# Kernel optimization log

Hardware: AMD Instinct MI355X
Metric: run time of the kernel (lower is better)

The kernel has to match this reference:

```python
import jax, jax.numpy as jnp
import numpy as np

NUM_CLASSES = 2
KS = 5  # kernel_size
EPS = 1e-8  # torch cosine_similarity eps


def setup_inputs() -> dict:
    key = jax.random.key(0)
    k1, k2, k3 = jax.random.split(key, 3)
    b, c, h, w = 8, 256, 128, 128
    er_input = jax.random.normal(k1, (b, c, h, w), dtype=jnp.float32)
    seg_label = jax.random.randint(k2, (b, h, w), 0, 2, dtype=jnp.int32)
    gt_boundary_seg = jax.random.randint(k3, (b, h, w), 0, 2, dtype=jnp.int32)
    return {"er_input": er_input, "seg_label": seg_label, "gt_boundary_seg": gt_boundary_seg}


def _context_loss(er_input, seg_label, gt_boundary_seg):
    # seg_label / gt_boundary_seg already at er_input spatial size (nearest interp is identity)
    b, c, h, w = er_input.shape
    r = KS // 2
    seg0 = jnp.where(seg_label == 255, 0, seg_label)
    gtb0 = jnp.where(gt_boundary_seg == 255, 0, gt_boundary_seg)
    gt_b = gtb0 * seg0                                  # [b,h,w] boundary pixels on fg classes
    interior = jnp.zeros((h, w), bool).at[r:h - r, r:w - r].set(True)
    valid = (gt_b > 0) & interior                       # pixels whose 5x5 window is in-bounds
    include = (gt_b > 0).any(axis=(1, 2))               # images contributing to scale_num
    cnt = valid.sum(axis=(1, 2)).astype(er_input.dtype)  # [b]

    norm = jnp.maximum(jnp.sqrt((er_input * er_input).sum(axis=1)), EPS)  # [b,h,w]
    validf = valid.astype(er_input.dtype)
    total = jnp.zeros((b,), dtype=er_input.dtype)
    n_shift = 0
    for dy in range(-r, r + 1):
        for dx in range(-r, r + 1):
            if dy == 0 and dx == 0:
                continue
            n_shift += 1
            # value at p+ (dy,dx) brought to p; valid pixels are interior so no wrap issue
            feat_s = jnp.roll(er_input, (-dy, -dx), axis=(2, 3))
            norm_s = jnp.roll(norm, (-dy, -dx), axis=(1, 2))
            seg_s = jnp.roll(seg_label, (-dy, -dx), axis=(1, 2))
            dot = (er_input * feat_s).sum(axis=1)       # [b,h,w]
            cos = dot / (norm * norm_s)
            # one_hot(seg,256)[:num_classes] dot product == labels equal AND label < num_classes
            labsim = ((seg_label == seg_s) & (seg_label < NUM_CLASSES)).astype(er_input.dtype)
            sq = (cos - labsim) ** 2
            # mse_loss over selected boundary pixels of image i
            total = total + (sq * validf).sum(axis=(1, 2)) / jnp.maximum(cnt, 1.0)
    loss_i = total / float(n_shift)                     # per-image context_loss_pi / 24
    scale_num = jnp.maximum(include.sum(), 1)
    return (loss_i * include.astype(loss_i.dtype)).sum() / scale_num.astype(loss_i.dtype)


def reference(er_input, seg_label, gt_boundary_seg):
    return _context_loss(er_input, seg_label, gt_boundary_seg)
```

## Files before the change

kernel.cpp:

```cpp
#include <hip/hip_runtime.h>
#include <math.h>

#define BATCH 8
#define CH    256
#define H     128
#define W     128
#define PLANE (H * W)
#define NPIX  (BATCH * PLANE)
#define NSHIFT 12
#define NMAPS  13
#define NCHUNK 8
#define CPC    (CH / NCHUNK)
#define SLICE  (NMAPS * NPIX)

static __device__ __constant__ int S_DY[NSHIFT] = {0,0,1,1,1,1,1,2,2,2,2,2};
static __device__ __constant__ int S_DX[NSHIFT] = {1,2,-2,-1,0,1,2,-2,-1,0,1,2};

#define NCORRB (BATCH * 32 * NCHUNK)
#define NSTATB (BATCH * 64)

__device__ __forceinline__ void fma4(float& acc, const float4& a, const float4& b) {
    acc = fmaf(a.x, b.x, acc);
    acc = fmaf(a.y, b.y, acc);
    acc = fmaf(a.z, b.z, acc);
    acc = fmaf(a.w, b.w, acc);
}

__global__ void k_prep(int* __restrict__ cnt, int* __restrict__ inc,
                       float* __restrict__ out) {
    int t = threadIdx.x;
    if (t < 8) { cnt[t] = 0; inc[t] = 0; }
    if (t == 0) out[0] = 0.0f;
}

__global__ __launch_bounds__(256) void k_corr(const float* __restrict__ er,
                                              const int* __restrict__ seg,
                                              const int* __restrict__ gtb,
                                              float* __restrict__ slices,
                                              int* __restrict__ cnt,
                                              int* __restrict__ inc) {
    __shared__ float4 lds[6][132];
    int t = threadIdx.x;

    if (blockIdx.x >= NCORRB) {
        int blk2 = blockIdx.x - NCORRB;
        int b = blk2 >> 6;
        int i = (blk2 & 63) * 256 + t;
        int my_cnt = 0, my_any = 0;
        {
            int s = seg[b * PLANE + i];
            int g = gtb[b * PLANE + i];
            int s0 = (s == 255) ? 0 : s;
            int g0 = (g == 255) ? 0 : g;
            if (s0 > 0 && g0 > 0) {
                my_any = 1;
                int y = i >> 7, x = i & 127;
                if (y >= 2 && y < H - 2 && x >= 2 && x < W - 2) my_cnt = 1;
            }
        }
        for (int o = 32; o > 0; o >>= 1) {
            my_cnt += __shfl_down(my_cnt, o, 64);
            my_any |= __shfl_down(my_any, o, 64);
        }
        __shared__ int sc[4], sa[4];
        int lane = t & 63, wid = t >> 6;
        if (lane == 0) { sc[wid] = my_cnt; sa[wid] = my_any; }
        __syncthreads();
        if (t == 0) {
            int c = sc[0] + sc[1] + sc[2] + sc[3];
            int a = sa[0] | sa[1] | sa[2] | sa[3];
            if (c) atomicAdd(&cnt[b], c);
            if (a) atomicOr(&inc[b], 1);
        }
        return;
    }

    int blk = blockIdx.x;
    int chunk = blk & 7;
    int tile  = (blk >> 3) & 31;
    int b     = blk >> 8;
    int y0 = tile * 4;
    int c0 = chunk * CPC;
    int r = t >> 7;
    int x = t & 127;

    if (t < 24) {
        int row = t >> 2, col = t & 3;
        int xs = (col < 2) ? col : (col + 128);
        lds[row][xs] = make_float4(0.f, 0.f, 0.f, 0.f);
    }

    float accA[13], accB[13];
#pragma unroll
    for (int i = 0; i < 13; i++) { accA[i] = 0.0f; accB[i] = 0.0f; }

    const float* base = er + (size_t)b * CH * PLANE;

    float pf[3][4];
    auto load_quad = [&](int c) {
#pragma unroll
        for (int k = 0; k < 3; ++k) {
            int s = t + k * 256;
            int row = s >> 7;
            int xs = s & 127;
            int y = y0 + row;
            if (y < H) {
                const float* p0 = base + (size_t)c * PLANE + y * W + xs;
                pf[k][0] = p0[0];
                pf[k][1] = p0[PLANE];
                pf[k][2] = p0[2 * PLANE];
                pf[k][3] = p0[3 * PLANE];
            } else {
                pf[k][0] = 0.f; pf[k][1] = 0.f; pf[k][2] = 0.f; pf[k][3] = 0.f;
            }
        }
    };

    load_quad(c0);
    const int iters = CPC / 4;
    for (int it = 0; it < iters; ++it) {
        __syncthreads();
#pragma unroll
        for (int k = 0; k < 3; ++k) {
            int s = t + k * 256;
            int row = s >> 7;
            int xs = s & 127;
            lds[row][xs + 2] = make_float4(pf[k][0], pf[k][1], pf[k][2], pf[k][3]);
        }
        __syncthreads();
        if (it + 1 < iters) load_quad(c0 + 4 * (it + 1));

        const float4* lp = &lds[2 * r][x + 2];
        float4 cA = lp[0];
        float4 cB = lp[132];
        {
            float4 v1 = lp[1], v2 = lp[2];
            fma4(accA[0], cA, cA);
            fma4(accA[1], cA, v1);
            fma4(accA[2], cA, v2);
        }
        {
            float4 m2 = lp[130], m1 = lp[131], p1 = lp[133], p2 = lp[134];
            fma4(accA[3], cA, m2);
            fma4(accA[4], cA, m1);
            fma4(accA[5], cA, cB);
            fma4(accA[6], cA, p1);
            fma4(accA[7], cA, p2);
            fma4(accB[0], cB, cB);
            fma4(accB[1], cB, p1);
            fma4(accB[2], cB, p2);
        }
        {
            float4 m2 = lp[262], m1 = lp[263], v0 = lp[264], p1 = lp[265], p2 = lp[266];
            fma4(accA[8],  cA, m2);
            fma4(accA[9],  cA, m1);
            fma4(accA[10], cA, v0);
            fma4(accA[11], cA, p1);
            fma4(accA[12], cA, p2);
            fma4(accB[3], cB, m2);
            fma4(accB[4], cB, m1);
            fma4(accB[5], cB, v0);
            fma4(accB[6], cB, p1);
            fma4(accB[7], cB, p2);
        }
        {
            float4 m2 = lp[394], m1 = lp[395], v0 = lp[396], p1 = lp[397], p2 = lp[398];
            fma4(accB[8],  cB, m2);
            fma4(accB[9],  cB, m1);
            fma4(accB[10], cB, v0);
            fma4(accB[11], cB, p1);
            fma4(accB[12], cB, p2);
        }
    }

    float* sp = slices + (size_t)chunk * SLICE;
    int pixA = b * PLANE + (y0 + 2 * r) * W + x;
    int pixB = pixA + W;
#pragma unroll
    for (int m = 0; m < NSHIFT; ++m) {
        sp[m * NPIX + pixA] = accA[m + 1];
        sp[m * NPIX + pixB] = accB[m + 1];
    }
    sp[NSHIFT * NPIX + pixA] = accA[0];
    sp[NSHIFT * NPIX + pixB] = accB[0];
}

__global__ __launch_bounds__(256) void k_combine(const float4* __restrict__ sl,
                                                 float4* __restrict__ comb) {
    int i = blockIdx.x * 256 + threadIdx.x;
    float4 s = sl[i];
#pragma unroll
    for (int c = 1; c < NCHUNK; ++c) {
        float4 v = sl[(size_t)c * (SLICE / 4) + i];
        s.x += v.x; s.y += v.y; s.z += v.z; s.w += v.w;
    }
    comb[i] = s;
}

__global__ __launch_bounds__(256) void k_loss(const float* __restrict__ comb,
                                              const int* __restrict__ seg,
                                              const int* __restrict__ gtb,
                                              const int* __restrict__ cnt,
                                              const int* __restrict__ inc,
                                              float* __restrict__ out) {
    const float* dots   = comb;
    const float* normsq = comb + NSHIFT * NPIX;
    int idx = blockIdx.x * 256 + threadIdx.x;
    int b = idx >> 14;
    int rem = idx & (PLANE - 1);
    int y = rem >> 7;
    int x = rem & 127;

    int sn = 0;
#pragma unroll
    for (int b2 = 0; b2 < BATCH; b2++) sn += (inc[b2] != 0);
    if (sn < 1) sn = 1;
    int cb = cnt[b]; if (cb < 1) cb = 1;
    float factor = inc[b] ? 1.0f / (24.0f * (float)cb * (float)sn) : 0.0f;

    float val = 0.0f;
    if (y >= 2 && y < H - 2 && x >= 2 && x < W - 2) {
        int sp = seg[idx];
        int gp = gtb[idx];
        int s0 = (sp == 255) ? 0 : sp;
        int g0 = (gp == 255) ? 0 : gp;
        if (s0 > 0 && g0 > 0) {
            float np = fmaxf(sqrtf(normsq[idx]), 1e-8f);
            float sum = 0.0f;
#pragma unroll
            for (int i = 0; i < NSHIFT; ++i) {
                int off = S_DY[i] * W + S_DX[i];
                {
                    float d  = dots[i * NPIX + idx];
                    float nn = fmaxf(sqrtf(normsq[idx + off]), 1e-8f);
                    float cosv = d / (np * nn);
                    int sq = seg[idx + off];
                    float lab = (sp == sq && sp < 2) ? 1.0f : 0.0f;
                    float tt = cosv - lab;
                    sum = fmaf(tt, tt, sum);
                }
                {
                    float d  = dots[i * NPIX + idx - off];
                    float nn = fmaxf(sqrtf(normsq[idx - off]), 1e-8f);
                    float cosv = d / (np * nn);
                    int sq = seg[idx - off];
                    float lab = (sp == sq && sp < 2) ? 1.0f : 0.0f;
                    float tt = cosv - lab;
                    sum = fmaf(tt, tt, sum);
                }
            }
            val = sum * factor;
        }
    }

    for (int o = 32; o > 0; o >>= 1)
        val += __shfl_down(val, o, 64);
    __shared__ float wsum[4];
    int lane = threadIdx.x & 63;
    int wid  = threadIdx.x >> 6;
    if (lane == 0) wsum[wid] = val;
    __syncthreads();
    if (threadIdx.x == 0) {
        float s = wsum[0] + wsum[1] + wsum[2] + wsum[3];
        atomicAdd(out, s);
    }
}

extern "C" void kernel_launch(void* const* d_in, const int* in_sizes, int n_in,
                              void* d_out, int out_size, void* d_ws, size_t ws_size,
                              hipStream_t stream) {
    const float* er  = (const float*)d_in[0];
    const int*   seg = (const int*)d_in[1];
    const int*   gtb = (const int*)d_in[2];
    float* out = (float*)d_out;

    float* ws     = (float*)d_ws;
    float* comb   = ws;
    float* slices = comb + SLICE;
    int*   cnt    = (int*)(slices + (size_t)NCHUNK * SLICE);
    int*   inc    = cnt + 8;

    hipLaunchKernelGGL(k_prep,    dim3(1), dim3(64), 0, stream, cnt, inc, out);
    hipLaunchKernelGGL(k_corr,    dim3(NCORRB + NSTATB), dim3(256), 0, stream,
                       er, seg, gtb, slices, cnt, inc);
    hipLaunchKernelGGL(k_combine, dim3(SLICE / 4 / 256), dim3(256), 0, stream,
                       (const float4*)slices, (float4*)comb);
    hipLaunchKernelGGL(k_loss,    dim3(NPIX / 256), dim3(256), 0, stream,
                       comb, seg, gtb, cnt, inc, out);
}
```

Measured before the change: 221.9 us.

## Restructure correlation kernel with LDS DMA loads and 4-pixel register blocking

The correlation kernel now stages two channels of a 10-row tile straight into LDS with global_load_lds, replacing register-staged quad loads. Each thread computes four horizontally adjacent pixels and reuses the loaded float4 neighbours across all shifts. Results are written back as float4 stores. The stats blocks become one per image that writes counts directly, which removes the separate zeroing kernel and the atomics. In exchange, the stage loop has no prefetch overlap, and edge columns and out-of-range rows read stale or neighbouring LDS data that only valid-masked pixels ignore.

```diff
diff --git a/kernel.cpp b/kernel.cpp
--- a/kernel.cpp
+++ b/kernel.cpp
@@ -1,5 +1,6 @@
 #include <hip/hip_runtime.h>
 #include <math.h>
+#include <stdint.h>
 
 #define BATCH 8
 #define CH    256
@@ -11,43 +12,40 @@
 #define NMAPS  13
 #define NCHUNK 8
 #define CPC    (CH / NCHUNK)
+#define NSTAGE (CPC / 2)
 #define SLICE  (NMAPS * NPIX)
+#define TROWS  8
+#define NTILE  (H / TROWS)
+#define NCORRB (BATCH * NTILE * NCHUNK)
+#define NSTATB (BATCH)
 
 static __device__ __constant__ int S_DY[NSHIFT] = {0,0,1,1,1,1,1,2,2,2,2,2};
 static __device__ __constant__ int S_DX[NSHIFT] = {1,2,-2,-1,0,1,2,-2,-1,0,1,2};
 
-#define NCORRB (BATCH * 32 * NCHUNK)
-#define NSTATB (BATCH * 64)
-
-__device__ __forceinline__ void fma4(float& acc, const float4& a, const float4& b) {
-    acc = fmaf(a.x, b.x, acc);
-    acc = fmaf(a.y, b.y, acc);
-    acc = fmaf(a.z, b.z, acc);
-    acc = fmaf(a.w, b.w, acc);
-}
-
-__global__ void k_prep(int* __restrict__ cnt, int* __restrict__ inc,
-                       float* __restrict__ out) {
+typedef unsigned int u32;
+
+__device__ __forceinline__ void dma16(const float* g, void* l) {
+    const __attribute__((address_space(1))) u32* gp =
+        (const __attribute__((address_space(1))) u32*)g;
+    __attribute__((address_space(3))) u32* lp =
+        (__attribute__((address_space(3))) u32*)(u32)(uintptr_t)l;
+    __builtin_amdgcn_global_load_lds(gp, lp, 16, 0, 0);
+}
+
+__global__ __launch_bounds__(256, 4) void k_corr(const float* __restrict__ er,
+                                                 const int* __restrict__ seg,
+                                                 const int* __restrict__ gtb,
+                                                 float* __restrict__ slices,
+                                                 int* __restrict__ cnt,
+                                                 int* __restrict__ inc,
+                                                 float* __restrict__ out) {
+    __shared__ float4 lds4[648];
     int t = threadIdx.x;
-    if (t < 8) { cnt[t] = 0; inc[t] = 0; }
-    if (t == 0) out[0] = 0.0f;
-}
-
-__global__ __launch_bounds__(256) void k_corr(const float* __restrict__ er,
-                                              const int* __restrict__ seg,
-                                              const int* __restrict__ gtb,
-                                              float* __restrict__ slices,
-                                              int* __restrict__ cnt,
-                                              int* __restrict__ inc) {
-    __shared__ float4 lds[6][132];
-    int t = threadIdx.x;
 
     if (blockIdx.x >= NCORRB) {
-        int blk2 = blockIdx.x - NCORRB;
-        int b = blk2 >> 6;
-        int i = (blk2 & 63) * 256 + t;
+        int b = blockIdx.x - NCORRB;
         int my_cnt = 0, my_any = 0;
-        {
+        for (int i = t; i < PLANE; i += 256) {
             int s = seg[b * PLANE + i];
             int g = gtb[b * PLANE + i];
             int s0 = (s == 255) ? 0 : s;
@@ -55,7 +53,7 @@
             if (s0 > 0 && g0 > 0) {
                 my_any = 1;
                 int y = i >> 7, x = i & 127;
-                if (y >= 2 && y < H - 2 && x >= 2 && x < W - 2) my_cnt = 1;
+                if (y >= 2 && y < H - 2 && x >= 2 && x < W - 2) my_cnt++;
             }
         }
         for (int o = 32; o > 0; o >>= 1) {
@@ -67,122 +65,91 @@
         if (lane == 0) { sc[wid] = my_cnt; sa[wid] = my_any; }
         __syncthreads();
         if (t == 0) {
-            int c = sc[0] + sc[1] + sc[2] + sc[3];
-            int a = sa[0] | sa[1] | sa[2] | sa[3];
-            if (c) atomicAdd(&cnt[b], c);
-            if (a) atomicOr(&inc[b], 1);
+            cnt[b] = sc[0] + sc[1] + sc[2] + sc[3];
+            inc[b] = sa[0] | sa[1] | sa[2] | sa[3];
+            if (b == 0) out[0] = 0.0f;
         }
         return;
     }
 
     int blk = blockIdx.x;
     int chunk = blk & 7;
-    int tile  = (blk >> 3) & 31;
-    int b     = blk >> 8;
-    int y0 = tile * 4;
+    int tile  = (blk >> 3) & 15;
+    int b     = blk >> 7;
+    int y0 = tile * TROWS;
     int c0 = chunk * CPC;
-    int r = t >> 7;
-    int x = t & 127;
-
-    if (t < 24) {
-        int row = t >> 2, col = t & 3;
-        int xs = (col < 2) ? col : (col + 128);
-        lds[row][xs] = make_float4(0.f, 0.f, 0.f, 0.f);
-    }
-
-    float accA[13], accB[13];
-#pragma unroll
-    for (int i = 0; i < 13; i++) { accA[i] = 0.0f; accB[i] = 0.0f; }
+    int q = t & 31;
+    int r = (t >> 5) & 7;
+    int w = t >> 6;
+    int ln = t & 63;
+
+    float accN[4], acc01[4], acc02[4], acc1[5][4], acc2[5][4];
+#pragma unroll
+    for (int j = 0; j < 4; ++j) {
+        accN[j] = 0.f; acc01[j] = 0.f; acc02[j] = 0.f;
+#pragma unroll
+        for (int d = 0; d < 5; ++d) { acc1[d][j] = 0.f; acc2[d][j] = 0.f; }
+    }
 
     const float* base = er + (size_t)b * CH * PLANE;
 
-    float pf[3][4];
-    auto load_quad = [&](int c) {
-#pragma unroll
-        for (int k = 0; k < 3; ++k) {
-            int s = t + k * 256;
-            int row = s >> 7;
-            int xs = s & 127;
-            int y = y0 + row;
-            if (y < H) {
-                const float* p0 = base + (size_t)c * PLANE + y * W + xs;
-                pf[k][0] = p0[0];
-                pf[k][1] = p0[PLANE];
-                pf[k][2] = p0[2 * PLANE];
-                pf[k][3] = p0[3 * PLANE];
-            } else {
-                pf[k][0] = 0.f; pf[k][1] = 0.f; pf[k][2] = 0.f; pf[k][3] = 0.f;
-            }
-        }
-    };
-
-    load_quad(c0);
-    const int iters = CPC / 4;
-    for (int it = 0; it < iters; ++it) {
+    for (int s = 0; s < NSTAGE; ++s) {
         __syncthreads();
-#pragma unroll
-        for (int k = 0; k < 3; ++k) {
-            int s = t + k * 256;
-            int row = s >> 7;
-            int xs = s & 127;
-            lds[row][xs + 2] = make_float4(pf[k][0], pf[k][1], pf[k][2], pf[k][3]);
+        const float* cb = base + (size_t)(c0 + 2 * s) * PLANE;
+#pragma unroll
+        for (int i = 0; i < 10; ++i) {
+            if ((i & 3) == w) {
+                int ch = i / 5, rp = i % 5;
+                int y = y0 + 2 * rp;
+                if (y < H) {
+                    const float* g = cb + (size_t)ch * PLANE + y * W + ln * 4;
+                    char* l = (char*)(lds4 + (ch * 10 + 2 * rp) * 32) + ln * 16;
+                    dma16(g, l);
+                }
+            }
         }
         __syncthreads();
-        if (it + 1 < iters) load_quad(c0 + 4 * (it + 1));
-
-        const float4* lp = &lds[2 * r][x + 2];
-        float4 cA = lp[0];
-        float4 cB = lp[132];
-        {
-            float4 v1 = lp[1], v2 = lp[2];
-            fma4(accA[0], cA, cA);
-            fma4(accA[1], cA, v1);
-            fma4(accA[2], cA, v2);
-        }
-        {
-            float4 m2 = lp[130], m1 = lp[131], p1 = lp[133], p2 = lp[134];
-            fma4(accA[3], cA, m2);
-            fma4(accA[4], cA, m1);
-            fma4(accA[5], cA, cB);
-            fma4(accA[6], cA, p1);
-            fma4(accA[7], cA, p2);
-            fma4(accB[0], cB, cB);
-            fma4(accB[1], cB, p1);
-            fma4(accB[2], cB, p2);
-        }
-        {
-            float4 m2 = lp[262], m1 = lp[263], v0 = lp[264], p1 = lp[265], p2 = lp[266];
-            fma4(accA[8],  cA, m2);
-            fma4(accA[9],  cA, m1);
-            fma4(accA[10], cA, v0);
-            fma4(accA[11], cA, p1);
-            fma4(accA[12], cA, p2);
-            fma4(accB[3], cB, m2);
-            fma4(accB[4], cB, m1);
-            fma4(accB[5], cB, v0);
-            fma4(accB[6], cB, p1);
-            fma4(accB[7], cB, p2);
-        }
-        {
-            float4 m2 = lp[394], m1 = lp[395], v0 = lp[396], p1 = lp[397], p2 = lp[398];
-            fma4(accB[8],  cB, m2);
-            fma4(accB[9],  cB, m1);
-            fma4(accB[10], cB, v0);
-            fma4(accB[11], cB, p1);
-            fma4(accB[12], cB, p2);
+
+#pragma unroll
+        for (int ch = 0; ch < 2; ++ch) {
+            const float4* Lrow = lds4 + (ch * 10 + r) * 32;
+            const float4* Mrow = Lrow + 32;
+            const float4* Nrow = Lrow + 64;
+            float4 A = Lrow[q], B = Lrow[q + 1];
+            float4 C4 = Mrow[q - 1], D4 = Mrow[q], E4 = Mrow[q + 1];
+            float4 F4 = Nrow[q - 1], G4 = Nrow[q], H4 = Nrow[q + 1];
+            float w8_[8] = {A.x, A.y, A.z, A.w, B.x, B.y, B.z, B.w};
+            float v_[12] = {C4.x, C4.y, C4.z, C4.w, D4.x, D4.y, D4.z, D4.w,
+                            E4.x, E4.y, E4.z, E4.w};
+            float u_[12] = {F4.x, F4.y, F4.z, F4.w, G4.x, G4.y, G4.z, G4.w,
+                            H4.x, H4.y, H4.z, H4.w};
+#pragma unroll
+            for (int j = 0; j < 4; ++j) {
+                float a = w8_[j];
+                accN[j]  = fmaf(a, a,          accN[j]);
+                acc01[j] = fmaf(a, w8_[j + 1], acc01[j]);
+                acc02[j] = fmaf(a, w8_[j + 2], acc02[j]);
+#pragma unroll
+                for (int d = 0; d < 5; ++d) {
+                    acc1[d][j] = fmaf(a, v_[j + d + 2], acc1[d][j]);
+                    acc2[d][j] = fmaf(a, u_[j + d + 2], acc2[d][j]);
+                }
+            }
         }
     }
 
     float* sp = slices + (size_t)chunk * SLICE;
-    int pixA = b * PLANE + (y0 + 2 * r) * W + x;
-    int pixB = pixA + W;
-#pragma unroll
-    for (int m = 0; m < NSHIFT; ++m) {
-        sp[m * NPIX + pixA] = accA[m + 1];
-        sp[m * NPIX + pixB] = accB[m + 1];
-    }
-    sp[NSHIFT * NPIX + pixA] = accA[0];
-    sp[NSHIFT * NPIX + pixB] = accB[0];
+    int pix = b * PLANE + (y0 + r) * W + 4 * q;
+    *(float4*)(sp + 0 * NPIX + pix) = make_float4(acc01[0], acc01[1], acc01[2], acc01[3]);
+    *(float4*)(sp + 1 * NPIX + pix) = make_float4(acc02[0], acc02[1], acc02[2], acc02[3]);
+#pragma unroll
+    for (int d = 0; d < 5; ++d) {
+        *(float4*)(sp + (2 + d) * NPIX + pix) =
+            make_float4(acc1[d][0], acc1[d][1], acc1[d][2], acc1[d][3]);
+        *(float4*)(sp + (7 + d) * NPIX + pix) =
+            make_float4(acc2[d][0], acc2[d][1], acc2[d][2], acc2[d][3]);
+    }
+    *(float4*)(sp + 12 * NPIX + pix) = make_float4(accN[0], accN[1], accN[2], accN[3]);
 }
 
 __global__ __launch_bounds__(256) void k_combine(const float4* __restrict__ sl,
@@ -280,9 +247,8 @@
     int*   cnt    = (int*)(slices + (size_t)NCHUNK * SLICE);
     int*   inc    = cnt + 8;
 
-    hipLaunchKernelGGL(k_prep,    dim3(1), dim3(64), 0, stream, cnt, inc, out);
     hipLaunchKernelGGL(k_corr,    dim3(NCORRB + NSTATB), dim3(256), 0, stream,
-                       er, seg, gtb, slices, cnt, inc);
+                       er, seg, gtb, slices, cnt, inc, out);
     hipLaunchKernelGGL(k_combine, dim3(SLICE / 4 / 256), dim3(256), 0, stream,
                        (const float4*)slices, (float4*)comb);
     hipLaunchKernelGGL(k_loss,    dim3(NPIX / 256), dim3(256), 0, stream,
```

New measurement: 269.0 us. 21.2% more time.

## Replace per-chunk slice buffers and combine pass with atomic accumulation

Applied to the files above, without the earlier changes.

The channel split drops from 8 to 4 chunks. Each chunk now atomically adds its partial dot products and squared norms straight into one zeroed accumulation buffer, and the separate combine kernel and the 8x slice buffers are gone. This cuts global write and read traffic for the partial maps and removes a launch. In exchange there is a zeroing pass, float atomics on every output, and non-deterministic summation order. The launch-bounds hint for occupancy is also added.

```diff
diff --git a/kernel.cpp b/kernel.cpp
--- a/kernel.cpp
+++ b/kernel.cpp
@@ -9,9 +9,9 @@
 #define NPIX  (BATCH * PLANE)
 #define NSHIFT 12
 #define NMAPS  13
-#define NCHUNK 8
+#define NCHUNK 4
 #define CPC    (CH / NCHUNK)
-#define SLICE  (NMAPS * NPIX)
+#define NZ4    (NMAPS * NPIX / 4)
 
 static __device__ __constant__ int S_DY[NSHIFT] = {0,0,1,1,1,1,1,2,2,2,2,2};
 static __device__ __constant__ int S_DX[NSHIFT] = {1,2,-2,-1,0,1,2,-2,-1,0,1,2};
@@ -26,19 +26,25 @@
     acc = fmaf(a.w, b.w, acc);
 }
 
-__global__ void k_prep(int* __restrict__ cnt, int* __restrict__ inc,
-                       float* __restrict__ out) {
-    int t = threadIdx.x;
-    if (t < 8) { cnt[t] = 0; inc[t] = 0; }
-    if (t == 0) out[0] = 0.0f;
-}
-
-__global__ __launch_bounds__(256) void k_corr(const float* __restrict__ er,
-                                              const int* __restrict__ seg,
-                                              const int* __restrict__ gtb,
-                                              float* __restrict__ slices,
+__global__ __launch_bounds__(256) void k_prep(float4* __restrict__ comb4,
                                               int* __restrict__ cnt,
-                                              int* __restrict__ inc) {
+                                              int* __restrict__ inc,
+                                              float* __restrict__ out) {
+    int i = blockIdx.x * 256 + threadIdx.x;
+    if (i < NZ4) comb4[i] = make_float4(0.f, 0.f, 0.f, 0.f);
+    if (blockIdx.x == 0) {
+        int t = threadIdx.x;
+        if (t < 8) { cnt[t] = 0; inc[t] = 0; }
+        if (t == 0) out[0] = 0.0f;
+    }
+}
+
+__global__ __launch_bounds__(256, 4) void k_corr(const float* __restrict__ er,
+                                                 const int* __restrict__ seg,
+                                                 const int* __restrict__ gtb,
+                                                 float* __restrict__ comb,
+                                                 int* __restrict__ cnt,
+                                                 int* __restrict__ inc) {
     __shared__ float4 lds[6][132];
     int t = threadIdx.x;
 
@@ -76,9 +82,9 @@
     }
 
     int blk = blockIdx.x;
-    int chunk = blk & 7;
-    int tile  = (blk >> 3) & 31;
-    int b     = blk >> 8;
+    int chunk = blk & 3;
+    int tile  = (blk >> 2) & 31;
+    int b     = blk >> 7;
     int y0 = tile * 4;
     int c0 = chunk * CPC;
     int r = t >> 7;
@@ -173,28 +179,15 @@
         }
     }
 
-    float* sp = slices + (size_t)chunk * SLICE;
     int pixA = b * PLANE + (y0 + 2 * r) * W + x;
     int pixB = pixA + W;
 #pragma unroll
     for (int m = 0; m < NSHIFT; ++m) {
-        sp[m * NPIX + pixA] = accA[m + 1];
-        sp[m * NPIX + pixB] = accB[m + 1];
-    }
-    sp[NSHIFT * NPIX + pixA] = accA[0];
-    sp[NSHIFT * NPIX + pixB] = accB[0];
-}
-
-__global__ __launch_bounds__(256) void k_combine(const float4* __restrict__ sl,
-                                                 float4* __restrict__ comb) {
-    int i = blockIdx.x * 256 + threadIdx.x;
-    float4 s = sl[i];
-#pragma unroll
-    for (int c = 1; c < NCHUNK; ++c) {
-        float4 v = sl[(size_t)c * (SLICE / 4) + i];
-        s.x += v.x; s.y += v.y; s.z += v.z; s.w += v.w;
-    }
-    comb[i] = s;
+        atomicAdd(&comb[m * NPIX + pixA], accA[m + 1]);
+        atomicAdd(&comb[m * NPIX + pixB], accB[m + 1]);
+    }
+    atomicAdd(&comb[NSHIFT * NPIX + pixA], accA[0]);
+    atomicAdd(&comb[NSHIFT * NPIX + pixB], accB[0]);
 }
 
 __global__ __launch_bounds__(256) void k_loss(const float* __restrict__ comb,
@@ -274,17 +267,15 @@
     const int*   gtb = (const int*)d_in[2];
     float* out = (float*)d_out;
 
-    float* ws     = (float*)d_ws;
-    float* comb   = ws;
-    float* slices = comb + SLICE;
-    int*   cnt    = (int*)(slices + (size_t)NCHUNK * SLICE);
-    int*   inc    = cnt + 8;
-
-    hipLaunchKernelGGL(k_prep,    dim3(1), dim3(64), 0, stream, cnt, inc, out);
-    hipLaunchKernelGGL(k_corr,    dim3(NCORRB + NSTATB), dim3(256), 0, stream,
-                       er, seg, gtb, slices, cnt, inc);
-    hipLaunchKernelGGL(k_combine, dim3(SLICE / 4 / 256), dim3(256), 0, stream,
-                       (const float4*)slices, (float4*)comb);
-    hipLaunchKernelGGL(k_loss,    dim3(NPIX / 256), dim3(256), 0, stream,
+    float* ws   = (float*)d_ws;
+    float* comb = ws;
+    int*   cnt  = (int*)(comb + NMAPS * NPIX);
+    int*   inc  = cnt + 8;
+
+    hipLaunchKernelGGL(k_prep, dim3((NZ4 + 255) / 256), dim3(256), 0, stream,
+                       (float4*)comb, cnt, inc, out);
+    hipLaunchKernelGGL(k_corr, dim3(NCORRB + NSTATB), dim3(256), 0, stream,
+                       er, seg, gtb, comb, cnt, inc);
+    hipLaunchKernelGGL(k_loss, dim3(NPIX / 256), dim3(256), 0, stream,
                        comb, seg, gtb, cnt, inc, out);
 }
```

Result: no change. 221.3 us (-0.3%).
